# Kernel optimization log

Measured on AMD Instinct MI355X. Metric: run time of the kernel, lower is better.

The kernel has to match this reference:

```python
import jax, jax.numpy as jnp
import numpy as np

NUM_EXPERTS = 64
TOP_K = 2


def setup_inputs() -> dict:
    key = jax.random.key(0)
    k1, k2 = jax.random.split(key)
    B, D, E = 16384, 4096, NUM_EXPERTS
    routing_features = jax.random.normal(k1, (B, D), dtype=jnp.float32)
    # nn.Linear(D, E, bias=False) weight: [E, D], kaiming-uniform-ish init
    bound = 1.0 / np.sqrt(D)
    gate_w = jax.random.uniform(k2, (E, D), dtype=jnp.float32, minval=-bound, maxval=bound)
    return {"routing_features": routing_features, "gate_w": gate_w}


def reference(routing_features, gate_w):
    B = routing_features.shape[0]
    E, K = NUM_EXPERTS, TOP_K
    # linear gate (no bias): [B, E]
    logits = jnp.einsum("bd,ed->be", routing_features, gate_w)
    full_probs = jax.nn.softmax(logits, axis=-1)
    top_k_logits, top_k_indices = jax.lax.top_k(logits, K)  # [B, K]
    top_k_weights = jax.nn.softmax(top_k_logits, axis=-1)
    # load-balance loss: f_i = fraction of (token, slot) assignments to expert i
    tokens_per_expert = jnp.zeros((E,), dtype=jnp.float32).at[top_k_indices.reshape(-1)].add(1.0)
    f = tokens_per_expert / (B * K)
    P = full_probs.mean(axis=0)
    aux_loss = E * jnp.sum(f * P)
    return top_k_weights, top_k_indices, aux_loss
```

## Files before the change

### kernel.cpp

```cpp
#include <hip/hip_runtime.h>
#include <math.h>


typedef __attribute__((ext_vector_type(8))) short bf16x8;
typedef __attribute__((ext_vector_type(4))) float f32x4;

constexpr int B_ROWS  = 16384;
constexpr int D_DIM   = 4096;
constexpr int E_EXP   = 64;
constexpr int TM      = 16;
constexpr int NTHR    = 512;
constexpr int NS      = 16;
constexpr int FLAGCAP = 8192;
constexpr float GAPTHR = 1e-3f;

__device__ __forceinline__ float wave_max64(float v) {
#pragma unroll
  for (int m = 32; m >= 1; m >>= 1) v = fmaxf(v, __shfl_xor(v, m, 64));
  return v;
}
__device__ __forceinline__ float wave_sum64(float v) {
#pragma unroll
  for (int m = 32; m >= 1; m >>= 1) v += __shfl_xor(v, m, 64);
  return v;
}
__device__ __forceinline__ void wave_argmax64(float v, int i, float& mv, int& mi) {
#pragma unroll
  for (int m = 32; m >= 1; m >>= 1) {
    float ov = __shfl_xor(v, m, 64);
    int   oi = __shfl_xor(i, m, 64);
    if (ov > v || (ov == v && oi < i)) { v = ov; i = oi; }
  }
  mv = v; mi = i;
}

__device__ __forceinline__ void split8(const f32x4 a, const f32x4 b, bf16x8& hi, bf16x8& lo) {
  float f[8] = {a[0], a[1], a[2], a[3], b[0], b[1], b[2], b[3]};
#pragma unroll
  for (int i = 0; i < 8; ++i) {
    unsigned int u = __float_as_uint(f[i]);
    hi[i] = (short)(u >> 16);
    float rem = f[i] - __uint_as_float(u & 0xffff0000u);
    lo[i] = (short)(__float_as_uint(rem) >> 16);
  }
}

__global__ __launch_bounds__(NTHR) void wsplit(const float* __restrict__ gw,
                                               char* __restrict__ wsW) {
  const int n = blockIdx.x;
  const int t = threadIdx.x;
  const int lane = t & 63, h = (t >> 6) & 1, wc = t >> 7;
  const int col = wc * 16 + (lane & 15);
  const int k0  = n * 32 + (lane >> 4) * 8;
  const float* src = gw + (size_t)col * D_DIM + k0;
  union { unsigned short us[8]; uint4 v; } pk;
#pragma unroll
  for (int i = 0; i < 8; ++i) {
    float f = src[i];
    unsigned int u = __float_as_uint(f);
    if (h == 0) {
      pk.us[i] = (unsigned short)(u >> 16);
    } else {
      float rem = f - __uint_as_float(u & 0xffff0000u);
      pk.us[i] = (unsigned short)(__float_as_uint(rem) >> 16);
    }
  }
  *(uint4*)(wsW + (size_t)n * 8192 + (size_t)t * 16) = pk.v;
}

__global__ __launch_bounds__(NTHR) void gemm_router(
    const float* __restrict__ rf, const char* __restrict__ wsW,
    float* __restrict__ out, float* __restrict__ psum,
    unsigned int* __restrict__ cnt, int* __restrict__ flagcnt,
    int* __restrict__ flaglist) {
  __shared__ char astrip[8][2][2048] __attribute__((aligned(16)));
  __shared__ float lt[TM][E_EXP + 2];
  __shared__ float pcol[E_EXP];
  __shared__ unsigned int scnt[E_EXP];

  const int t = threadIdx.x, lane = t & 63, wv = t >> 6;
  const int row0 = blockIdx.x * TM;

  for (int i = t; i < TM * (E_EXP + 2); i += NTHR) ((float*)lt)[i] = 0.f;
  if (t < E_EXP) { scnt[t] = 0; pcol[t] = 0.f; }
  __syncthreads();

  const int rW = lane >> 2;
  const int sW = (lane & 3) * 2;
  const int xW = rW & 7;
  const float* gsrc = rf + (size_t)(row0 + rW) * D_DIM + wv * (NS * 32) + sW * 4;
  char* mystrip = &astrip[wv][0][0];
  const int wo0 = rW * 128 + (((sW)     ^ xW) << 4);
  const int wo1 = rW * 128 + (((sW + 1) ^ xW) << 4);

  const int rr = lane & 15;
  const int s0 = (lane >> 4) * 2;
  const int ro0 = rr * 128 + (((s0) ^ (rr & 7)) << 4);
  const int ro1 = ro0 ^ 16;

  const char* wbase = wsW + (size_t)(wv * NS) * 8192 + (size_t)lane * 16;

  f32x4 acc[4] = {{0.f,0.f,0.f,0.f},{0.f,0.f,0.f,0.f},{0.f,0.f,0.f,0.f},{0.f,0.f,0.f,0.f}};
  f32x4 aR0, aR1;

  auto G = [&](int n) {
    aR0 = *(const f32x4*)(gsrc + n * 32);
    aR1 = *(const f32x4*)(gsrc + n * 32 + 4);
  };
  auto DSW = [&](int slot) {
    char* s = mystrip + slot * 2048;
    *(f32x4*)(s + wo0) = aR0;
    *(f32x4*)(s + wo1) = aR1;
  };

  G(0); DSW(0);
  G(1);
#pragma unroll 2
  for (int n = 0; n < NS; ++n) {
    if (n + 1 < NS) DSW((n + 1) & 1);
    if (n + 2 < NS) G(n + 2);
    const char* s = mystrip + (n & 1) * 2048;
    f32x4 fl = *(const f32x4*)(s + ro0);
    f32x4 fh = *(const f32x4*)(s + ro1);
    bf16x8 ahi, alo;
    split8(fl, fh, ahi, alo);
    const char* wn = wbase + (size_t)n * 8192;
#pragma unroll
    for (int cb = 0; cb < 4; ++cb) {
      bf16x8 whi = *(const bf16x8*)(wn + cb * 2048);
      bf16x8 wlo = *(const bf16x8*)(wn + cb * 2048 + 1024);
      acc[cb] = __builtin_amdgcn_mfma_f32_16x16x32_bf16(ahi, whi, acc[cb], 0, 0, 0);
      acc[cb] = __builtin_amdgcn_mfma_f32_16x16x32_bf16(ahi, wlo, acc[cb], 0, 0, 0);
      acc[cb] = __builtin_amdgcn_mfma_f32_16x16x32_bf16(alo, whi, acc[cb], 0, 0, 0);
      acc[cb] = __builtin_amdgcn_mfma_f32_16x16x32_bf16(alo, wlo, acc[cb], 0, 0, 0);
    }
  }

  {
    const int colb = lane & 15;
    const int rowb = (lane >> 4) * 4;
#pragma unroll
    for (int cb = 0; cb < 4; ++cb)
#pragma unroll
      for (int j = 0; j < 4; ++j)
        atomicAdd(&lt[rowb + j][cb * 16 + colb], acc[cb][j]);
  }
  __syncthreads();

#pragma unroll
  for (int j = 0; j < 2; ++j) {
    const int r = wv * 2 + j;
    const float lg = lt[r][lane];
    const float m  = wave_max64(lg);
    const float p  = __expf(lg - m);
    const float ss = wave_sum64(p);
    atomicAdd(&pcol[lane], p / ss);
    float v1; int i1; wave_argmax64(lg, lane, v1, i1);
    const float lm1 = (lane == i1) ? -INFINITY : lg;
    float v2; int i2; wave_argmax64(lm1, lane, v2, i2);
    const float lm2 = (lane == i2) ? -INFINITY : lm1;
    float v3; int i3; wave_argmax64(lm2, lane, v3, i3);
    if (lane == 0) {
      const float ex = expf(v2 - v1);
      const int row = row0 + r;
      out[row * 2 + 0] = 1.f / (1.f + ex);
      out[row * 2 + 1] = ex / (1.f + ex);
      out[2 * B_ROWS + row * 2 + 0] = (float)i1;
      out[2 * B_ROWS + row * 2 + 1] = (float)i2;
      atomicAdd(&scnt[i1], 1u);
      atomicAdd(&scnt[i2], 1u);
      if (v1 - v2 < GAPTHR || v2 - v3 < GAPTHR) {
        int fi = atomicAdd(flagcnt, 1);
        if (fi < FLAGCAP) flaglist[fi] = row;
      }
    }
  }
  __syncthreads();
  if (t < E_EXP) {
    atomicAdd(&psum[t], pcol[t]);
    const unsigned int c = scnt[t];
    if (c) atomicAdd(&cnt[t], c);
  }
}

__global__ __launch_bounds__(256) void cleanup(
    const float* __restrict__ rf, const float* __restrict__ gw,
    const int* __restrict__ flagcnt, const int* __restrict__ flaglist,
    float* __restrict__ out) {
  __shared__ double sm[256];
  const int t = threadIdx.x;
  const int nf = min(*flagcnt, FLAGCAP);
  for (int fi = blockIdx.x; fi < nf; fi += gridDim.x) {
    const int row = flaglist[fi];
    const int e = t & 63, seg = t >> 6;
    const float* a = rf + (size_t)row * D_DIM + seg * 1024;
    const float* w = gw + (size_t)e * D_DIM + seg * 1024;
    double p0 = 0.0, p1 = 0.0, p2 = 0.0, p3 = 0.0;
    for (int k = 0; k < 1024; k += 4) {
      p0 = fma((double)a[k + 0], (double)w[k + 0], p0);
      p1 = fma((double)a[k + 1], (double)w[k + 1], p1);
      p2 = fma((double)a[k + 2], (double)w[k + 2], p2);
      p3 = fma((double)a[k + 3], (double)w[k + 3], p3);
    }
    sm[t] = (p0 + p1) + (p2 + p3);
    __syncthreads();
    if (t < 64) {
      const double l = sm[t] + sm[64 + t] + sm[128 + t] + sm[192 + t];
      double v = l; int ii = t;
#pragma unroll
      for (int m = 32; m >= 1; m >>= 1) {
        double ov = __shfl_xor(v, m, 64); int oi = __shfl_xor(ii, m, 64);
        if (ov > v || (ov == v && oi < ii)) { v = ov; ii = oi; }
      }
      const double v1 = v; const int i1 = ii;
      const double lm = (t == i1) ? -1e300 : l;
      v = lm; ii = t;
#pragma unroll
      for (int m = 32; m >= 1; m >>= 1) {
        double ov = __shfl_xor(v, m, 64); int oi = __shfl_xor(ii, m, 64);
        if (ov > v || (ov == v && oi < ii)) { v = ov; ii = oi; }
      }
      const double v2 = v; const int i2 = ii;
      if (t == 0) {
        const double ex = exp(v2 - v1);
        out[row * 2 + 0] = (float)(1.0 / (1.0 + ex));
        out[row * 2 + 1] = (float)(ex / (1.0 + ex));
        out[2 * B_ROWS + row * 2 + 0] = (float)i1;
        out[2 * B_ROWS + row * 2 + 1] = (float)i2;
      }
    }
    __syncthreads();
  }
}

__global__ void aux_finalize(const float* __restrict__ psum,
                             const unsigned int* __restrict__ cnt,
                             float* __restrict__ out) {
  const int t = threadIdx.x;
  const float f = (float)cnt[t] / (float)(B_ROWS * 2);
  const float P = psum[t] / (float)B_ROWS;
  float v = f * P;
  v = wave_sum64(v);
  if (t == 0) out[4 * B_ROWS] = (float)E_EXP * v;
}

extern "C" void kernel_launch(void* const* d_in, const int* in_sizes, int n_in,
                              void* d_out, int out_size, void* d_ws, size_t ws_size,
                              hipStream_t stream) {
  const float* rf = (const float*)d_in[0];
  const float* gw = (const float*)d_in[1];
  float* out = (float*)d_out;
  float* psum = (float*)d_ws;
  unsigned int* cnt = (unsigned int*)((char*)d_ws + 256);
  int* flagcnt = (int*)((char*)d_ws + 512);
  int* flaglist = (int*)((char*)d_ws + 768);
  char* wsW = (char*)d_ws + 65536;

  hipMemsetAsync(d_ws, 0, 768, stream);
  wsplit<<<D_DIM / 32, NTHR, 0, stream>>>(gw, wsW);
  gemm_router<<<B_ROWS / TM, NTHR, 0, stream>>>(rf, wsW, out, psum, cnt,
                                                flagcnt, flaglist);
  cleanup<<<64, 256, 0, stream>>>(rf, gw, flagcnt, flaglist, out);
  aux_finalize<<<1, 64, 0, stream>>>(psum, cnt, out);
}
```

Before: 230.5 us.

## Load A fragments directly to registers, double-buffer weights, drop lo*lo MFMA

Removes the LDS staging strip for the activation tile. Each lane now loads its MFMA A-fragment straight from global memory, and both the A fragments and the bf16 weight fragments are double-buffered in registers two k-steps ahead. The alo*wlo MFMA term of the split-bf16 emulation is also dropped, cutting matrix work per step from 4 to 3 MFMAs. The cost is more register pressure, less coalesced global reads of the activations, and slightly lower precision in the logits, which could change top-k picks near ties.

```diff
diff --git a/kernel.cpp b/kernel.cpp
--- a/kernel.cpp
+++ b/kernel.cpp
@@ -73,7 +73,6 @@
     float* __restrict__ out, float* __restrict__ psum,
     unsigned int* __restrict__ cnt, int* __restrict__ flagcnt,
     int* __restrict__ flaglist) {
-  __shared__ char astrip[8][2][2048] __attribute__((aligned(16)));
   __shared__ float lt[TM][E_EXP + 2];
   __shared__ float pcol[E_EXP];
   __shared__ unsigned int scnt[E_EXP];
@@ -85,56 +84,60 @@
   if (t < E_EXP) { scnt[t] = 0; pcol[t] = 0.f; }
   __syncthreads();
 
-  const int rW = lane >> 2;
-  const int sW = (lane & 3) * 2;
-  const int xW = rW & 7;
-  const float* gsrc = rf + (size_t)(row0 + rW) * D_DIM + wv * (NS * 32) + sW * 4;
-  char* mystrip = &astrip[wv][0][0];
-  const int wo0 = rW * 128 + (((sW)     ^ xW) << 4);
-  const int wo1 = rW * 128 + (((sW + 1) ^ xW) << 4);
-
-  const int rr = lane & 15;
-  const int s0 = (lane >> 4) * 2;
-  const int ro0 = rr * 128 + (((s0) ^ (rr & 7)) << 4);
-  const int ro1 = ro0 ^ 16;
-
+  const float* aptr = rf + (size_t)(row0 + (lane & 15)) * D_DIM
+                         + wv * (NS * 32) + (lane >> 4) * 8;
   const char* wbase = wsW + (size_t)(wv * NS) * 8192 + (size_t)lane * 16;
 
   f32x4 acc[4] = {{0.f,0.f,0.f,0.f},{0.f,0.f,0.f,0.f},{0.f,0.f,0.f,0.f},{0.f,0.f,0.f,0.f}};
-  f32x4 aR0, aR1;
-
-  auto G = [&](int n) {
-    aR0 = *(const f32x4*)(gsrc + n * 32);
-    aR1 = *(const f32x4*)(gsrc + n * 32 + 4);
-  };
-  auto DSW = [&](int slot) {
-    char* s = mystrip + slot * 2048;
-    *(f32x4*)(s + wo0) = aR0;
-    *(f32x4*)(s + wo1) = aR1;
-  };
-
-  G(0); DSW(0);
-  G(1);
-#pragma unroll 2
-  for (int n = 0; n < NS; ++n) {
-    if (n + 1 < NS) DSW((n + 1) & 1);
-    if (n + 2 < NS) G(n + 2);
-    const char* s = mystrip + (n & 1) * 2048;
-    f32x4 fl = *(const f32x4*)(s + ro0);
-    f32x4 fh = *(const f32x4*)(s + ro1);
-    bf16x8 ahi, alo;
-    split8(fl, fh, ahi, alo);
-    const char* wn = wbase + (size_t)n * 8192;
-#pragma unroll
-    for (int cb = 0; cb < 4; ++cb) {
-      bf16x8 whi = *(const bf16x8*)(wn + cb * 2048);
-      bf16x8 wlo = *(const bf16x8*)(wn + cb * 2048 + 1024);
-      acc[cb] = __builtin_amdgcn_mfma_f32_16x16x32_bf16(ahi, whi, acc[cb], 0, 0, 0);
-      acc[cb] = __builtin_amdgcn_mfma_f32_16x16x32_bf16(ahi, wlo, acc[cb], 0, 0, 0);
-      acc[cb] = __builtin_amdgcn_mfma_f32_16x16x32_bf16(alo, whi, acc[cb], 0, 0, 0);
-      acc[cb] = __builtin_amdgcn_mfma_f32_16x16x32_bf16(alo, wlo, acc[cb], 0, 0, 0);
-    }
-  }
+
+  f32x4 aA0, aA1, aB0, aB1;
+  bf16x8 wAhi[4], wAlo[4], wBhi[4], wBlo[4];
+
+#define LDA_A(n) { aA0 = *(const f32x4*)(aptr + (n) * 32); \
+                   aA1 = *(const f32x4*)(aptr + (n) * 32 + 4); }
+#define LDA_B(n) { aB0 = *(const f32x4*)(aptr + (n) * 32); \
+                   aB1 = *(const f32x4*)(aptr + (n) * 32 + 4); }
+#define LDW_A(n) { const char* wn_ = wbase + (size_t)(n) * 8192; \
+    _Pragma("unroll") for (int cb = 0; cb < 4; ++cb) { \
+      wAhi[cb] = *(const bf16x8*)(wn_ + cb * 2048); \
+      wAlo[cb] = *(const bf16x8*)(wn_ + cb * 2048 + 1024); } }
+#define LDW_B(n) { const char* wn_ = wbase + (size_t)(n) * 8192; \
+    _Pragma("unroll") for (int cb = 0; cb < 4; ++cb) { \
+      wBhi[cb] = *(const bf16x8*)(wn_ + cb * 2048); \
+      wBlo[cb] = *(const bf16x8*)(wn_ + cb * 2048 + 1024); } }
+
+  LDA_A(0); LDW_A(0);
+  LDA_B(1); LDW_B(1);
+  for (int n = 0; n < NS; n += 2) {
+    {
+      bf16x8 ahi, alo;
+      split8(aA0, aA1, ahi, alo);
+      if (n + 2 < NS) LDA_A(n + 2);
+#pragma unroll
+      for (int cb = 0; cb < 4; ++cb) {
+        acc[cb] = __builtin_amdgcn_mfma_f32_16x16x32_bf16(ahi, wAhi[cb], acc[cb], 0, 0, 0);
+        acc[cb] = __builtin_amdgcn_mfma_f32_16x16x32_bf16(alo, wAhi[cb], acc[cb], 0, 0, 0);
+        acc[cb] = __builtin_amdgcn_mfma_f32_16x16x32_bf16(ahi, wAlo[cb], acc[cb], 0, 0, 0);
+      }
+      if (n + 2 < NS) LDW_A(n + 2);
+    }
+    {
+      bf16x8 ahi, alo;
+      split8(aB0, aB1, ahi, alo);
+      if (n + 3 < NS) LDA_B(n + 3);
+#pragma unroll
+      for (int cb = 0; cb < 4; ++cb) {
+        acc[cb] = __builtin_amdgcn_mfma_f32_16x16x32_bf16(ahi, wBhi[cb], acc[cb], 0, 0, 0);
+        acc[cb] = __builtin_amdgcn_mfma_f32_16x16x32_bf16(alo, wBhi[cb], acc[cb], 0, 0, 0);
+        acc[cb] = __builtin_amdgcn_mfma_f32_16x16x32_bf16(ahi, wBlo[cb], acc[cb], 0, 0, 0);
+      }
+      if (n + 3 < NS) LDW_B(n + 3);
+    }
+  }
+#undef LDA_A
+#undef LDA_B
+#undef LDW_A
+#undef LDW_B
 
   {
     const int colb = lane & 15;
```

New measurement: 236.6 us. 2.6% more time.
